# Kernel optimization log

Hardware: AMD Instinct MI355X
Metric: run time of the kernel (lower is better)

The kernel has to match this reference:

```python
import jax, jax.numpy as jnp
import numpy as np

INPUT_DIM = 1024
EMBED_DIM = 256


def setup_inputs() -> dict:
    key = jax.random.key(0)
    ks = jax.random.split(key, 7)
    s_in = 1.0 / np.sqrt(INPUT_DIM)
    x = jax.random.normal(ks[0], (4, 2048, INPUT_DIM), dtype=jnp.float32)
    Wq = jax.random.uniform(ks[1], (INPUT_DIM, EMBED_DIM), jnp.float32, -s_in, s_in)
    bq = jax.random.uniform(ks[2], (EMBED_DIM,), jnp.float32, -s_in, s_in)
    Wk = jax.random.uniform(ks[3], (INPUT_DIM, EMBED_DIM), jnp.float32, -s_in, s_in)
    bk = jax.random.uniform(ks[4], (EMBED_DIM,), jnp.float32, -s_in, s_in)
    Wv = jax.random.uniform(ks[5], (INPUT_DIM, EMBED_DIM), jnp.float32, -s_in, s_in)
    bv = jax.random.uniform(ks[6], (EMBED_DIM,), jnp.float32, -s_in, s_in)
    return {"x": x, "Wq": Wq, "bq": bq, "Wk": Wk, "bk": bk, "Wv": Wv, "bv": bv}


def reference(x, Wq, bq, Wk, bk, Wv, bv):
    # B,T,C -> single-head attention. NOTE: original multiplies by C**0.5.
    C = x.shape[-1]
    scale = jnp.asarray(C, x.dtype) ** 0.5
    q = jnp.einsum('btc,ce->bte', x, Wq) + bq  # [B,T,E]
    k = jnp.einsum('btc,ce->bte', x, Wk) + bk
    v = jnp.einsum('btc,ce->bte', x, Wv) + bv
    wei = jnp.einsum('bqe,bke->bqk', q, k) * scale  # [B,T,T]
    wei = jax.nn.softmax(wei, axis=-1)
    # dropout p=0.0 (eval): identity
    out = jnp.einsum('bqk,bke->bqe', wei, v)  # [B,T,E]
    return out
```

## Files before the change

### kernel.cpp

```cpp
#include <hip/hip_runtime.h>
#include <math.h>

#define IDIM 1024
#define EDIM 256
#define NB 4
#define NT 2048
#define NROW 8192

typedef __attribute__((ext_vector_type(8))) short short8;
typedef __attribute__((ext_vector_type(4))) float f32x4;

#define MFMA16(A,B,C) __builtin_amdgcn_mfma_f32_16x16x32_bf16(A,B,C,0,0,0)
#define GLD16(gsrc, ldst) __builtin_amdgcn_global_load_lds( \
    (const __attribute__((address_space(1))) unsigned int*)(gsrc), \
    (__attribute__((address_space(3))) unsigned int*)(ldst), 16, 0, 0)

__device__ __forceinline__ unsigned short f2bf(float x){
    unsigned u = __builtin_bit_cast(unsigned, x);
    u += 0x7fffu + ((u >> 16) & 1u);
    return (unsigned short)(u >> 16);
}
__device__ __forceinline__ float bf2f(unsigned short h){
    unsigned u = ((unsigned)h) << 16;
    return __builtin_bit_cast(float, u);
}

__global__ __launch_bounds__(256) void split_x(
    const float* __restrict__ X, ushort* __restrict__ Xh, ushort* __restrict__ Xl)
{
    size_t i = ((size_t)blockIdx.x * 256 + threadIdx.x) * 8;
    float4 a = *(const float4*)(X + i);
    float4 b = *(const float4*)(X + i + 4);
    float v[8] = {a.x, a.y, a.z, a.w, b.x, b.y, b.z, b.w};
    union { ushort us[8]; uint4 u; } hi, lo;
    #pragma unroll
    for (int j = 0; j < 8; ++j) {
        unsigned short h = f2bf(v[j]);
        hi.us[j] = h;
        lo.us[j] = f2bf(v[j] - bf2f(h));
    }
    *(uint4*)(Xh + i) = hi.u;
    *(uint4*)(Xl + i) = lo.u;
}

__global__ __launch_bounds__(256) void split_w(
    const float* __restrict__ Wq, const float* __restrict__ Wk, const float* __restrict__ Wv,
    ushort* __restrict__ Wqh, ushort* __restrict__ Wql,
    ushort* __restrict__ Wkh, ushort* __restrict__ Wkl,
    ushort* __restrict__ Wvh)
{
    int u = blockIdx.x * 256 + threadIdx.x;
    int z   = u >> 15;
    int rem = u & 32767;
    int ko  = rem >> 8;
    int e   = rem & 255;
    const float* W = (z == 0) ? Wq : (z == 1) ? Wk : Wv;
    ushort* Oh = (z == 0) ? Wqh : (z == 1) ? Wkh : Wvh;
    ushort* Ol = (z == 0) ? Wql : Wkl;
    union { ushort us[8]; uint4 v; } hi, lo;
    #pragma unroll
    for (int j = 0; j < 8; ++j) {
        float wv = W[(size_t)(ko * 8 + j) * 256 + e];
        unsigned short h = f2bf(wv);
        hi.us[j] = h;
        lo.us[j] = f2bf(wv - bf2f(h));
    }
    *(uint4*)(Oh + (size_t)e * 1024 + ko * 8) = hi.v;
    if (z < 2) *(uint4*)(Ol + (size_t)e * 1024 + ko * 8) = lo.v;
}

__global__ __launch_bounds__(256) void qkv_proj(
    const ushort* __restrict__ Xh, const ushort* __restrict__ Xl,
    const ushort* __restrict__ Whq, const ushort* __restrict__ Wlq,
    const ushort* __restrict__ Whk, const ushort* __restrict__ Wlk,
    const ushort* __restrict__ Whv,
    const float* __restrict__ bq, const float* __restrict__ bk, const float* __restrict__ bv,
    ushort* __restrict__ Qh, ushort* __restrict__ Ql,
    ushort* __restrict__ Kh, ushort* __restrict__ Kl,
    ushort* __restrict__ Vt)
{
    __shared__ ushort Ah[4096], Al[4096], Bh[4096], Bl[4096];

    const int tid = threadIdx.x;
    const int lane = tid & 63, w = tid >> 6;
    const int ln = tid & 15, quad = (tid >> 4) & 3;
    const int wr = w >> 1, wc = w & 1;
    const int z = blockIdx.z;
    const int n0 = blockIdx.x * 128, m0 = blockIdx.y * 128;
    const ushort* Wh = (z == 0) ? Whq : (z == 1) ? Whk : Whv;
    const ushort* Wl = (z == 0) ? Wlq : Wlk;

    f32x4 acc[4][4];
    #pragma unroll
    for (int mi = 0; mi < 4; ++mi)
        #pragma unroll
        for (int ni = 0; ni < 4; ++ni) acc[mi][ni] = (f32x4){0.f, 0.f, 0.f, 0.f};

    const ushort* a0 = Xh + (size_t)(m0 + lane) * IDIM + w * 8;
    const ushort* a1 = Xh + (size_t)(m0 + 64 + lane) * IDIM + w * 8;
    const ushort* a0l = Xl + (size_t)(m0 + lane) * IDIM + w * 8;
    const ushort* a1l = Xl + (size_t)(m0 + 64 + lane) * IDIM + w * 8;
    const ushort* b0 = Wh + (size_t)(n0 + lane) * IDIM + w * 8;
    const ushort* b1 = Wh + (size_t)(n0 + 64 + lane) * IDIM + w * 8;
    const ushort* b0l = Wl + (size_t)(n0 + lane) * IDIM + w * 8;
    const ushort* b1l = Wl + (size_t)(n0 + 64 + lane) * IDIM + w * 8;
    ushort* dA0 = Ah + (size_t)(w * 128) * 8;
    ushort* dA1 = Ah + (size_t)(w * 128 + 64) * 8;
    ushort* dA0l = Al + (size_t)(w * 128) * 8;
    ushort* dA1l = Al + (size_t)(w * 128 + 64) * 8;
    ushort* dB0 = Bh + (size_t)(w * 128) * 8;
    ushort* dB1 = Bh + (size_t)(w * 128 + 64) * 8;
    ushort* dB0l = Bl + (size_t)(w * 128) * 8;
    ushort* dB1l = Bl + (size_t)(w * 128 + 64) * 8;

    for (int kk = 0; kk < IDIM; kk += 32) {
        GLD16(a0 + kk, dA0);
        GLD16(a1 + kk, dA1);
        GLD16(b0 + kk, dB0);
        GLD16(b1 + kk, dB1);
        if (z < 2) {
            GLD16(a0l + kk, dA0l);
            GLD16(a1l + kk, dA1l);
            GLD16(b0l + kk, dB0l);
            GLD16(b1l + kk, dB1l);
        }
        __syncthreads();

        short8 ah[4], al[4], bh[4], bl[4];
        #pragma unroll
        for (int mi = 0; mi < 4; ++mi) {
            int au = quad * 128 + wr * 64 + mi * 16 + ln;
            ah[mi] = *(const short8*)(Ah + au * 8);
            if (z < 2) al[mi] = *(const short8*)(Al + au * 8);
        }
        #pragma unroll
        for (int ni = 0; ni < 4; ++ni) {
            int bu = quad * 128 + wc * 64 + ni * 16 + ln;
            bh[ni] = *(const short8*)(Bh + bu * 8);
            if (z < 2) bl[ni] = *(const short8*)(Bl + bu * 8);
        }
        if (z < 2) {
            #pragma unroll
            for (int ni = 0; ni < 4; ++ni)
                #pragma unroll
                for (int mi = 0; mi < 4; ++mi) {
                    acc[mi][ni] = MFMA16(ah[mi], bh[ni], acc[mi][ni]);
                    acc[mi][ni] = MFMA16(ah[mi], bl[ni], acc[mi][ni]);
                    acc[mi][ni] = MFMA16(al[mi], bh[ni], acc[mi][ni]);
                }
        } else {
            #pragma unroll
            for (int ni = 0; ni < 4; ++ni)
                #pragma unroll
                for (int mi = 0; mi < 4; ++mi)
                    acc[mi][ni] = MFMA16(ah[mi], bh[ni], acc[mi][ni]);
        }
        __syncthreads();
    }

    if (z < 2) {
        ushort* OH = (z == 0) ? Qh : Kh;
        ushort* OL = (z == 0) ? Ql : Kl;
        const float* bias = (z == 0) ? bq : bk;
        const float scale = (z == 0) ? 46.16624130844683f : 1.0f;
        #pragma unroll
        for (int ni = 0; ni < 4; ++ni) {
            int col = n0 + wc * 64 + ni * 16 + ln;
            float bb = bias[col];
            #pragma unroll
            for (int mi = 0; mi < 4; ++mi)
                #pragma unroll
                for (int r = 0; r < 4; ++r) {
                    int row = m0 + wr * 64 + mi * 16 + quad * 4 + r;
                    float v = (acc[mi][ni][r] + bb) * scale;
                    unsigned short hh = f2bf(v);
                    OH[(size_t)row * EDIM + col] = hh;
                    OL[(size_t)row * EDIM + col] = f2bf(v - bf2f(hh));
                }
        }
    } else {
        #pragma unroll
        for (int ni = 0; ni < 4; ++ni) {
            int col = n0 + wc * 64 + ni * 16 + ln;
            float bb = bv[col];
            #pragma unroll
            for (int mi = 0; mi < 4; ++mi) {
                int rowb = m0 + wr * 64 + mi * 16 + quad * 4;
                union { ushort us[4]; uint2 v; } pk;
                #pragma unroll
                for (int r = 0; r < 4; ++r) pk.us[r] = f2bf(acc[mi][ni][r] + bb);
                *(uint2*)(Vt + (size_t)col * NROW + rowb) = pk.v;
            }
        }
    }
}

__global__ __launch_bounds__(256, 2) void attn(
    const ushort* __restrict__ Qh, const ushort* __restrict__ Ql,
    const ushort* __restrict__ Kh, const ushort* __restrict__ Kl,
    const ushort* __restrict__ Vt, ushort* __restrict__ Op, float* __restrict__ mlbuf)
{
    __shared__ ushort KVbuf[4096];
    __shared__ ushort Qls[16384];
    __shared__ ushort Pall[4 * 1088];

    const int tid = threadIdx.x;
    const int lane = tid & 63;
    const int ln = tid & 15, quad = (tid >> 4) & 3, w = tid >> 6;
    ushort* Qls_w = Qls + w * 4096;
    ushort* Pw = Pall + w * 1088;

    const int id = blockIdx.x;
    const int cls = id & 15;
    const int b = cls >> 2, kvq = cls & 3;
    const int qt = id >> 4;
    const int qrow0w = b * NT + qt * 64 + w * 16;
    const int kvbase = b * NT + kvq * 512;

    short8 qh8[8];
    #pragma unroll
    for (int kc = 0; kc < 8; ++kc)
        qh8[kc] = *(const short8*)(Qh + (size_t)(qrow0w + ln) * EDIM + kc * 32 + quad * 8);
    #pragma unroll
    for (int i = 0; i < 8; ++i) {
        int u = i * 64 + lane;
        int ko = u >> 4, ln2 = u & 15;
        *(uint4*)(Qls_w + u * 8) =
            *(const uint4*)(Ql + (size_t)(qrow0w + ln2) * EDIM + ko * 8);
    }

    float m_r[4], l_r[4];
    #pragma unroll
    for (int r = 0; r < 4; ++r) { m_r[r] = -3e38f; l_r[r] = 0.f; }
    f32x4 o[16];
    #pragma unroll
    for (int ni = 0; ni < 16; ++ni) o[ni] = (f32x4){0.f, 0.f, 0.f, 0.f};

    for (int t = 0; t < 8; ++t) {
        const int kv0 = kvbase + t * 64;
        f32x4 s[4];
        #pragma unroll
        for (int ni = 0; ni < 4; ++ni) s[ni] = (f32x4){0.f, 0.f, 0.f, 0.f};

        #pragma unroll
        for (int kc = 0; kc < 8; ++kc) {
            size_t goff = (size_t)(kv0 + w * 16 + (lane & 15)) * EDIM
                          + kc * 32 + (lane >> 4) * 8;
            GLD16(Kh + goff, KVbuf + w * 512);
            GLD16(Kl + goff, KVbuf + 2048 + w * 512);
            __syncthreads();
            short8 ql8 = *(const short8*)(Qls_w + ((kc * 4 + quad) * 16 + ln) * 8);
            #pragma unroll
            for (int ni = 0; ni < 4; ++ni) {
                short8 bh = *(const short8*)(KVbuf + (ni * 64 + quad * 16 + ln) * 8);
                short8 bl = *(const short8*)(KVbuf + 2048 + (ni * 64 + quad * 16 + ln) * 8);
                s[ni] = MFMA16(qh8[kc], bh, s[ni]);
                s[ni] = MFMA16(qh8[kc], bl, s[ni]);
                s[ni] = MFMA16(ql8, bh, s[ni]);
            }
            __syncthreads();
        }

        float mt[4];
        #pragma unroll
        for (int r = 0; r < 4; ++r)
            mt[r] = fmaxf(fmaxf(s[0][r], s[1][r]), fmaxf(s[2][r], s[3][r]));
        #pragma unroll
        for (int mask = 1; mask < 16; mask <<= 1)
            #pragma unroll
            for (int r = 0; r < 4; ++r)
                mt[r] = fmaxf(mt[r], __shfl_xor(mt[r], mask));
        float alpha[4];
        #pragma unroll
        for (int r = 0; r < 4; ++r) {
            float mn = fmaxf(m_r[r], mt[r]);
            alpha[r] = exp2f(m_r[r] - mn);
            m_r[r] = mn;
        }
        float ls[4] = {0.f, 0.f, 0.f, 0.f};
        #pragma unroll
        for (int ni = 0; ni < 4; ++ni) {
            int colb = ni * 16 + ln;
            #pragma unroll
            for (int r = 0; r < 4; ++r) {
                float p = exp2f(s[ni][r] - m_r[r]);
                ls[r] += p;
                Pw[((colb >> 3) * 17 + quad * 4 + r) * 8 + (colb & 7)] = f2bf(p);
            }
        }
        #pragma unroll
        for (int mask = 1; mask < 16; mask <<= 1)
            #pragma unroll
            for (int r = 0; r < 4; ++r)
                ls[r] += __shfl_xor(ls[r], mask);
        #pragma unroll
        for (int r = 0; r < 4; ++r) l_r[r] = l_r[r] * alpha[r] + ls[r];
        #pragma unroll
        for (int ni = 0; ni < 16; ++ni)
            #pragma unroll
            for (int r = 0; r < 4; ++r) o[ni][r] *= alpha[r];

        short8 apk0 = *(const short8*)(Pw + (quad * 17 + ln) * 8);
        short8 apk1 = *(const short8*)(Pw + ((4 + quad) * 17 + ln) * 8);
        #pragma unroll
        for (int vs = 0; vs < 4; ++vs) {
            size_t gv = (size_t)(vs * 64 + w * 16 + (lane & 15)) * NROW
                        + kv0 + (lane >> 4) * 8;
            GLD16(Vt + gv, KVbuf + w * 1024);
            GLD16(Vt + gv + 32, KVbuf + w * 1024 + 512);
            __syncthreads();
            #pragma unroll
            for (int ni = 0; ni < 4; ++ni) {
                short8 v0 = *(const short8*)(KVbuf + (ni * 128 + quad * 16 + ln) * 8);
                short8 v1 = *(const short8*)(KVbuf + (ni * 128 + 64 + quad * 16 + ln) * 8);
                o[vs * 4 + ni] = MFMA16(apk0, v0, o[vs * 4 + ni]);
                o[vs * 4 + ni] = MFMA16(apk1, v1, o[vs * 4 + ni]);
            }
            __syncthreads();
        }
    }

    const int p = (b * 32 + qt) * 4 + kvq;
    if (ln == 0) {
        #pragma unroll
        for (int r = 0; r < 4; ++r) {
            int row = w * 16 + quad * 4 + r;
            *(float2*)(mlbuf + ((size_t)p * 64 + row) * 2) = make_float2(m_r[r], l_r[r]);
        }
    }
    #pragma unroll
    for (int ni = 0; ni < 16; ++ni)
        #pragma unroll
        for (int r = 0; r < 4; ++r) {
            int row = w * 16 + quad * 4 + r;
            Op[(size_t)p * 16384 + row * 256 + ni * 16 + ln] = f2bf(o[ni][r]);
        }
}

__global__ __launch_bounds__(256) void attn_merge(
    const ushort* __restrict__ Op, const float* __restrict__ mlbuf, float* __restrict__ out)
{
    const int bid = blockIdx.x, t = threadIdx.x;
    const int b = bid >> 7, qt = (bid >> 2) & 31, rg = bid & 3;
    const int row = rg * 16 + (t >> 4);
    const int e0 = (t & 15) * 16;
    const int pb = (b * 32 + qt) * 4;
    float mv[4], lv[4];
    float M = -3e38f;
    #pragma unroll
    for (int w2 = 0; w2 < 4; ++w2) {
        float2 ml = *(const float2*)(mlbuf + ((size_t)(pb + w2) * 64 + row) * 2);
        mv[w2] = ml.x; lv[w2] = ml.y;
        M = fmaxf(M, ml.x);
    }
    float sc[4], denom = 0.f;
    #pragma unroll
    for (int w2 = 0; w2 < 4; ++w2) {
        sc[w2] = exp2f(mv[w2] - M);
        denom += sc[w2] * lv[w2];
    }
    float inv = 1.0f / denom;
    #pragma unroll
    for (int w2 = 0; w2 < 4; ++w2) sc[w2] *= inv;

    float acc[16] = {};
    #pragma unroll
    for (int w2 = 0; w2 < 4; ++w2) {
        const ushort* src = Op + (size_t)(pb + w2) * 16384 + row * 256 + e0;
        #pragma unroll
        for (int c = 0; c < 2; ++c) {
            union { ushort us[8]; uint4 v; } u;
            u.v = *(const uint4*)(src + c * 8);
            #pragma unroll
            for (int j = 0; j < 8; ++j)
                acc[c * 8 + j] += sc[w2] * bf2f(u.us[j]);
        }
    }
    float* op = out + ((size_t)b * NT + qt * 64 + row) * EDIM + e0;
    #pragma unroll
    for (int g = 0; g < 4; ++g)
        *(float4*)(op + g * 4) = make_float4(acc[g*4], acc[g*4+1], acc[g*4+2], acc[g*4+3]);
}

extern "C" void kernel_launch(void* const* d_in, const int* in_sizes, int n_in,
                              void* d_out, int out_size, void* d_ws, size_t ws_size,
                              hipStream_t stream) {
    const float* x  = (const float*)d_in[0];
    const float* Wq = (const float*)d_in[1];
    const float* bq = (const float*)d_in[2];
    const float* Wk = (const float*)d_in[3];
    const float* bk = (const float*)d_in[4];
    const float* Wv = (const float*)d_in[5];
    const float* bv = (const float*)d_in[6];
    float* out = (float*)d_out;

    const size_t NX = (size_t)NROW * IDIM;
    const size_t NE = (size_t)NB * NT * EDIM;
    ushort* Xh = (ushort*)d_ws;
    ushort* Xl = Xh + NX;
    ushort* Qh = Xl + NX;
    ushort* Ql = Qh + NE;
    ushort* Kh = Ql + NE;
    ushort* Kl = Kh + NE;
    ushort* Vt = Kl + NE;
    ushort* Wqh = Vt + NE;
    ushort* Wql = Wqh + 256 * 1024;
    ushort* Wkh = Wql + 256 * 1024;
    ushort* Wkl = Wkh + 256 * 1024;
    ushort* Wvh = Wkl + 256 * 1024;
    ushort* Op  = Xh;
    float*  mlb = (float*)(Xh + (size_t)512 * 16384);

    split_x<<<4096, 256, 0, stream>>>(x, Xh, Xl);
    split_w<<<384, 256, 0, stream>>>(Wq, Wk, Wv, Wqh, Wql, Wkh, Wkl, Wvh);
    qkv_proj<<<dim3(2, 64, 3), 256, 0, stream>>>(Xh, Xl, Wqh, Wql, Wkh, Wkl, Wvh,
                                                 bq, bk, bv, Qh, Ql, Kh, Kl, Vt);
    attn<<<512, 256, 0, stream>>>(Qh, Ql, Kh, Kl, Vt, Op, mlb);
    attn_merge<<<512, 256, 0, stream>>>(Op, mlb, out);
}
```

Before: 233.7 us.

## Rewrite attention kernel with 32x32 MFMA tiles and per-tile K/V staging

The attention kernel now runs 2 waves per block, each owning 32 query rows, and uses 32x32x16 bf16 MFMA instead of 16x16x32. Each 32-key tile of K hi/lo and V is loaded into LDS with a single barrier per tile, replacing the per-k-chunk loads and barriers, and the Q hi/lo fragments stay in registers. The aim is to cut synchronisation and LDS staging overhead and to raise MFMA efficiency. In exchange, register pressure rises sharply (two 16-entry Q fragment sets plus 8 f32x16 accumulators), occupancy drops, and the softmax now does a full 32-lane reduction per row. qkv_proj also gets a launch-bounds occupancy hint.

```diff
diff --git a/kernel.cpp b/kernel.cpp
--- a/kernel.cpp
+++ b/kernel.cpp
@@ -9,8 +9,10 @@
 
 typedef __attribute__((ext_vector_type(8))) short short8;
 typedef __attribute__((ext_vector_type(4))) float f32x4;
+typedef __attribute__((ext_vector_type(16))) float f32x16;
 
 #define MFMA16(A,B,C) __builtin_amdgcn_mfma_f32_16x16x32_bf16(A,B,C,0,0,0)
+#define MFMA32(A,B,C) __builtin_amdgcn_mfma_f32_32x32x16_bf16(A,B,C,0,0,0)
 #define GLD16(gsrc, ldst) __builtin_amdgcn_global_load_lds( \
     (const __attribute__((address_space(1))) unsigned int*)(gsrc), \
     (__attribute__((address_space(3))) unsigned int*)(ldst), 16, 0, 0)
@@ -69,7 +71,7 @@
     if (z < 2) *(uint4*)(Ol + (size_t)e * 1024 + ko * 8) = lo.v;
 }
 
-__global__ __launch_bounds__(256) void qkv_proj(
+__global__ __launch_bounds__(256, 2) void qkv_proj(
     const ushort* __restrict__ Xh, const ushort* __restrict__ Xl,
     const ushort* __restrict__ Whq, const ushort* __restrict__ Wlq,
     const ushort* __restrict__ Whk, const ushort* __restrict__ Wlk,
@@ -195,146 +197,141 @@
     }
 }
 
-__global__ __launch_bounds__(256, 2) void attn(
+__global__ __launch_bounds__(128, 1) void attn(
     const ushort* __restrict__ Qh, const ushort* __restrict__ Ql,
     const ushort* __restrict__ Kh, const ushort* __restrict__ Kl,
     const ushort* __restrict__ Vt, ushort* __restrict__ Op, float* __restrict__ mlbuf)
 {
-    __shared__ ushort KVbuf[4096];
-    __shared__ ushort Qls[16384];
-    __shared__ ushort Pall[4 * 1088];
+    __shared__ ushort KhiL[8192];
+    __shared__ ushort KloL[8192];
+    __shared__ ushort VsL[8192];
+    __shared__ ushort Pall[2 * 1152];
 
     const int tid = threadIdx.x;
-    const int lane = tid & 63;
-    const int ln = tid & 15, quad = (tid >> 4) & 3, w = tid >> 6;
-    ushort* Qls_w = Qls + w * 4096;
-    ushort* Pw = Pall + w * 1088;
+    const int lane = tid & 63, w = tid >> 6;
+    const int lm = lane & 31, hh = lane >> 5;
+    ushort* Pw = Pall + w * 1152;
 
     const int id = blockIdx.x;
     const int cls = id & 15;
     const int b = cls >> 2, kvq = cls & 3;
     const int qt = id >> 4;
-    const int qrow0w = b * NT + qt * 64 + w * 16;
+    const int qrow0w = b * NT + qt * 64 + w * 32;
     const int kvbase = b * NT + kvq * 512;
 
-    short8 qh8[8];
-    #pragma unroll
-    for (int kc = 0; kc < 8; ++kc)
-        qh8[kc] = *(const short8*)(Qh + (size_t)(qrow0w + ln) * EDIM + kc * 32 + quad * 8);
-    #pragma unroll
-    for (int i = 0; i < 8; ++i) {
-        int u = i * 64 + lane;
-        int ko = u >> 4, ln2 = u & 15;
-        *(uint4*)(Qls_w + u * 8) =
-            *(const uint4*)(Ql + (size_t)(qrow0w + ln2) * EDIM + ko * 8);
-    }
-
-    float m_r[4], l_r[4];
-    #pragma unroll
-    for (int r = 0; r < 4; ++r) { m_r[r] = -3e38f; l_r[r] = 0.f; }
-    f32x4 o[16];
-    #pragma unroll
-    for (int ni = 0; ni < 16; ++ni) o[ni] = (f32x4){0.f, 0.f, 0.f, 0.f};
-
-    for (int t = 0; t < 8; ++t) {
-        const int kv0 = kvbase + t * 64;
-        f32x4 s[4];
-        #pragma unroll
-        for (int ni = 0; ni < 4; ++ni) s[ni] = (f32x4){0.f, 0.f, 0.f, 0.f};
-
-        #pragma unroll
-        for (int kc = 0; kc < 8; ++kc) {
-            size_t goff = (size_t)(kv0 + w * 16 + (lane & 15)) * EDIM
-                          + kc * 32 + (lane >> 4) * 8;
-            GLD16(Kh + goff, KVbuf + w * 512);
-            GLD16(Kl + goff, KVbuf + 2048 + w * 512);
-            __syncthreads();
-            short8 ql8 = *(const short8*)(Qls_w + ((kc * 4 + quad) * 16 + ln) * 8);
-            #pragma unroll
-            for (int ni = 0; ni < 4; ++ni) {
-                short8 bh = *(const short8*)(KVbuf + (ni * 64 + quad * 16 + ln) * 8);
-                short8 bl = *(const short8*)(KVbuf + 2048 + (ni * 64 + quad * 16 + ln) * 8);
-                s[ni] = MFMA16(qh8[kc], bh, s[ni]);
-                s[ni] = MFMA16(qh8[kc], bl, s[ni]);
-                s[ni] = MFMA16(ql8, bh, s[ni]);
-            }
-            __syncthreads();
-        }
-
-        float mt[4];
-        #pragma unroll
-        for (int r = 0; r < 4; ++r)
-            mt[r] = fmaxf(fmaxf(s[0][r], s[1][r]), fmaxf(s[2][r], s[3][r]));
-        #pragma unroll
-        for (int mask = 1; mask < 16; mask <<= 1)
-            #pragma unroll
-            for (int r = 0; r < 4; ++r)
-                mt[r] = fmaxf(mt[r], __shfl_xor(mt[r], mask));
-        float alpha[4];
-        #pragma unroll
-        for (int r = 0; r < 4; ++r) {
-            float mn = fmaxf(m_r[r], mt[r]);
+    short8 qh[16], ql[16];
+    #pragma unroll
+    for (int kc = 0; kc < 16; ++kc) {
+        size_t qoff = (size_t)(qrow0w + lm) * EDIM + kc * 16 + hh * 8;
+        qh[kc] = *(const short8*)(Qh + qoff);
+        ql[kc] = *(const short8*)(Ql + qoff);
+    }
+
+    float m_r[16], l_r[16];
+    #pragma unroll
+    for (int r = 0; r < 16; ++r) { m_r[r] = -3e38f; l_r[r] = 0.f; }
+    f32x16 o[8];
+    #pragma unroll
+    for (int eb = 0; eb < 8; ++eb)
+        #pragma unroll
+        for (int r = 0; r < 16; ++r) o[eb][r] = 0.f;
+
+    #pragma unroll 1
+    for (int t = 0; t < 16; ++t) {
+        const int kv0 = kvbase + t * 32;
+
+        #pragma unroll
+        for (int j = 0; j < 8; ++j) {
+            int u = (w * 8 + j) * 64 + lane;
+            int eo = u >> 5, c = u & 31;
+            size_t koff = (size_t)(kv0 + c) * EDIM + eo * 8;
+            GLD16(Kh + koff, KhiL + (size_t)(w * 8 + j) * 512);
+            GLD16(Kl + koff, KloL + (size_t)(w * 8 + j) * 512);
+        }
+        #pragma unroll
+        for (int j = 0; j < 8; ++j) {
+            int u = (w * 8 + j) * 64 + lane;
+            int koct = u >> 8, e = u & 255;
+            GLD16(Vt + (size_t)e * NROW + kv0 + koct * 8,
+                  VsL + (size_t)(w * 8 + j) * 512);
+        }
+        __syncthreads();
+
+        f32x16 s;
+        #pragma unroll
+        for (int r = 0; r < 16; ++r) s[r] = 0.f;
+        #pragma unroll
+        for (int kc = 0; kc < 16; ++kc) {
+            int bu = (kc * 2 + hh) * 32 + lm;
+            short8 bh = *(const short8*)(KhiL + bu * 8);
+            short8 bl = *(const short8*)(KloL + bu * 8);
+            s = MFMA32(qh[kc], bh, s);
+            s = MFMA32(qh[kc], bl, s);
+            s = MFMA32(ql[kc], bh, s);
+        }
+
+        float alpha[16], p[16];
+        #pragma unroll
+        for (int r = 0; r < 16; ++r) {
+            float mt = s[r];
+            #pragma unroll
+            for (int mask = 1; mask < 32; mask <<= 1)
+                mt = fmaxf(mt, __shfl_xor(mt, mask));
+            float mn = fmaxf(m_r[r], mt);
             alpha[r] = exp2f(m_r[r] - mn);
             m_r[r] = mn;
-        }
-        float ls[4] = {0.f, 0.f, 0.f, 0.f};
-        #pragma unroll
-        for (int ni = 0; ni < 4; ++ni) {
-            int colb = ni * 16 + ln;
-            #pragma unroll
-            for (int r = 0; r < 4; ++r) {
-                float p = exp2f(s[ni][r] - m_r[r]);
-                ls[r] += p;
-                Pw[((colb >> 3) * 17 + quad * 4 + r) * 8 + (colb & 7)] = f2bf(p);
+            float pv = exp2f(s[r] - mn);
+            p[r] = pv;
+            float ls = pv;
+            #pragma unroll
+            for (int mask = 1; mask < 32; mask <<= 1)
+                ls += __shfl_xor(ls, mask);
+            l_r[r] = l_r[r] * alpha[r] + ls;
+        }
+        #pragma unroll
+        for (int rg = 0; rg < 4; ++rg) {
+            union { ushort us[4]; uint2 v; } pk;
+            #pragma unroll
+            for (int r4 = 0; r4 < 4; ++r4) pk.us[r4] = f2bf(p[rg * 4 + r4]);
+            *(uint2*)(Pw + lm * 36 + rg * 8 + hh * 4) = pk.v;
+        }
+        #pragma unroll
+        for (int eb = 0; eb < 8; ++eb)
+            #pragma unroll
+            for (int r = 0; r < 16; ++r) o[eb][r] *= alpha[r];
+
+        #pragma unroll
+        for (int c = 0; c < 2; ++c) {
+            short8 ap;
+            #pragma unroll
+            for (int j = 0; j < 8; ++j)
+                ((ushort*)&ap)[j] = Pw[(c * 16 + hh * 8 + j) * 36 + lm];
+            #pragma unroll
+            for (int eb = 0; eb < 8; ++eb) {
+                short8 bv8 = *(const short8*)(VsL +
+                    ((size_t)(c * 2 + hh) * 256 + eb * 32 + lm) * 8);
+                o[eb] = MFMA32(ap, bv8, o[eb]);
             }
         }
-        #pragma unroll
-        for (int mask = 1; mask < 16; mask <<= 1)
-            #pragma unroll
-            for (int r = 0; r < 4; ++r)
-                ls[r] += __shfl_xor(ls[r], mask);
-        #pragma unroll
-        for (int r = 0; r < 4; ++r) l_r[r] = l_r[r] * alpha[r] + ls[r];
-        #pragma unroll
-        for (int ni = 0; ni < 16; ++ni)
-            #pragma unroll
-            for (int r = 0; r < 4; ++r) o[ni][r] *= alpha[r];
-
-        short8 apk0 = *(const short8*)(Pw + (quad * 17 + ln) * 8);
-        short8 apk1 = *(const short8*)(Pw + ((4 + quad) * 17 + ln) * 8);
-        #pragma unroll
-        for (int vs = 0; vs < 4; ++vs) {
-            size_t gv = (size_t)(vs * 64 + w * 16 + (lane & 15)) * NROW
-                        + kv0 + (lane >> 4) * 8;
-            GLD16(Vt + gv, KVbuf + w * 1024);
-            GLD16(Vt + gv + 32, KVbuf + w * 1024 + 512);
-            __syncthreads();
-            #pragma unroll
-            for (int ni = 0; ni < 4; ++ni) {
-                short8 v0 = *(const short8*)(KVbuf + (ni * 128 + quad * 16 + ln) * 8);
-                short8 v1 = *(const short8*)(KVbuf + (ni * 128 + 64 + quad * 16 + ln) * 8);
-                o[vs * 4 + ni] = MFMA16(apk0, v0, o[vs * 4 + ni]);
-                o[vs * 4 + ni] = MFMA16(apk1, v1, o[vs * 4 + ni]);
-            }
-            __syncthreads();
-        }
-    }
-
-    const int p = (b * 32 + qt) * 4 + kvq;
-    if (ln == 0) {
-        #pragma unroll
-        for (int r = 0; r < 4; ++r) {
-            int row = w * 16 + quad * 4 + r;
-            *(float2*)(mlbuf + ((size_t)p * 64 + row) * 2) = make_float2(m_r[r], l_r[r]);
-        }
-    }
-    #pragma unroll
-    for (int ni = 0; ni < 16; ++ni)
-        #pragma unroll
-        for (int r = 0; r < 4; ++r) {
-            int row = w * 16 + quad * 4 + r;
-            Op[(size_t)p * 16384 + row * 256 + ni * 16 + ln] = f2bf(o[ni][r]);
-        }
+        __syncthreads();
+    }
+
+    const int pi = (b * 32 + qt) * 4 + kvq;
+    if (lm == 0) {
+        #pragma unroll
+        for (int r = 0; r < 16; ++r) {
+            int row = w * 32 + (r & 3) + 8 * (r >> 2) + 4 * hh;
+            *(float2*)(mlbuf + ((size_t)pi * 64 + row) * 2) = make_float2(m_r[r], l_r[r]);
+        }
+    }
+    #pragma unroll
+    for (int r = 0; r < 16; ++r) {
+        int row = w * 32 + (r & 3) + 8 * (r >> 2) + 4 * hh;
+        ushort* dst = Op + (size_t)pi * 16384 + row * 256 + lm;
+        #pragma unroll
+        for (int eb = 0; eb < 8; ++eb)
+            dst[eb * 32] = f2bf(o[eb][r]);
+    }
 }
 
 __global__ __launch_bounds__(256) void attn_merge(
@@ -415,6 +412,6 @@
     split_w<<<384, 256, 0, stream>>>(Wq, Wk, Wv, Wqh, Wql, Wkh, Wkl, Wvh);
     qkv_proj<<<dim3(2, 64, 3), 256, 0, stream>>>(Xh, Xl, Wqh, Wql, Wkh, Wkl, Wvh,
                                                  bq, bk, bv, Qh, Ql, Kh, Kl, Vt);
-    attn<<<512, 256, 0, stream>>>(Qh, Ql, Kh, Kl, Vt, Op, mlb);
+    attn<<<512, 128, 0, stream>>>(Qh, Ql, Kh, Kl, Vt, Op, mlb);
     attn_merge<<<512, 256, 0, stream>>>(Op, mlb, out);
 }
```

New measurement: 299.6 us. 1.28x slower.

## Stage whole K/V tile per step in attention, cutting barriers per iteration

Applied to the files above, without the earlier changes.

The attention kernel now loads a full 32-key tile of K-hi, K-lo and V into shared memory once per step with a single barrier, instead of staging small chunks with two barriers each. Q-lo fragments are held in registers rather than LDS, and the KV step shrinks from 64 to 32 keys. This is meant to cut synchronisation and LDS traffic, at the cost of more LDS per block, more registers and twice as many softmax rescale steps. The projection kernel also gets a launch bound of two blocks per CU.

```diff
diff --git a/kernel.cpp b/kernel.cpp
--- a/kernel.cpp
+++ b/kernel.cpp
@@ -69,7 +69,7 @@
     if (z < 2) *(uint4*)(Ol + (size_t)e * 1024 + ko * 8) = lo.v;
 }
 
-__global__ __launch_bounds__(256) void qkv_proj(
+__global__ __launch_bounds__(256, 2) void qkv_proj(
     const ushort* __restrict__ Xh, const ushort* __restrict__ Xl,
     const ushort* __restrict__ Whq, const ushort* __restrict__ Wlq,
     const ushort* __restrict__ Whk, const ushort* __restrict__ Wlk,
@@ -200,15 +200,14 @@
     const ushort* __restrict__ Kh, const ushort* __restrict__ Kl,
     const ushort* __restrict__ Vt, ushort* __restrict__ Op, float* __restrict__ mlbuf)
 {
-    __shared__ ushort KVbuf[4096];
-    __shared__ ushort Qls[16384];
-    __shared__ ushort Pall[4 * 1088];
+    __shared__ ushort KhiL[8192];
+    __shared__ ushort KloL[8192];
+    __shared__ ushort VsL[8192];
+    __shared__ ushort Pall[4 * 544];
 
     const int tid = threadIdx.x;
-    const int lane = tid & 63;
     const int ln = tid & 15, quad = (tid >> 4) & 3, w = tid >> 6;
-    ushort* Qls_w = Qls + w * 4096;
-    ushort* Pw = Pall + w * 1088;
+    ushort* Pw = Pall + w * 544;
 
     const int id = blockIdx.x;
     const int cls = id & 15;
@@ -217,16 +216,12 @@
     const int qrow0w = b * NT + qt * 64 + w * 16;
     const int kvbase = b * NT + kvq * 512;
 
-    short8 qh8[8];
-    #pragma unroll
-    for (int kc = 0; kc < 8; ++kc)
-        qh8[kc] = *(const short8*)(Qh + (size_t)(qrow0w + ln) * EDIM + kc * 32 + quad * 8);
-    #pragma unroll
-    for (int i = 0; i < 8; ++i) {
-        int u = i * 64 + lane;
-        int ko = u >> 4, ln2 = u & 15;
-        *(uint4*)(Qls_w + u * 8) =
-            *(const uint4*)(Ql + (size_t)(qrow0w + ln2) * EDIM + ko * 8);
+    short8 qh8[8], ql8[8];
+    #pragma unroll
+    for (int kc = 0; kc < 8; ++kc) {
+        size_t qoff = (size_t)(qrow0w + ln) * EDIM + kc * 32 + quad * 8;
+        qh8[kc] = *(const short8*)(Qh + qoff);
+        ql8[kc] = *(const short8*)(Ql + qoff);
     }
 
     float m_r[4], l_r[4];
@@ -236,35 +231,46 @@
     #pragma unroll
     for (int ni = 0; ni < 16; ++ni) o[ni] = (f32x4){0.f, 0.f, 0.f, 0.f};
 
-    for (int t = 0; t < 8; ++t) {
-        const int kv0 = kvbase + t * 64;
-        f32x4 s[4];
-        #pragma unroll
-        for (int ni = 0; ni < 4; ++ni) s[ni] = (f32x4){0.f, 0.f, 0.f, 0.f};
-
+    #pragma unroll 1
+    for (int t = 0; t < 16; ++t) {
+        const int kv0 = kvbase + t * 32;
+
+        #pragma unroll
+        for (int r = 0; r < 4; ++r) {
+            int u = r * 256 + tid;
+            int c = u & 31, kq = u >> 5;
+            size_t ksrc = (size_t)(kv0 + c) * EDIM + kq * 8;
+            GLD16(Kh + ksrc, KhiL + (size_t)(r * 256 + (tid & ~63)) * 8);
+            GLD16(Kl + ksrc, KloL + (size_t)(r * 256 + (tid & ~63)) * 8);
+        }
+        #pragma unroll
+        for (int r = 0; r < 4; ++r) {
+            int u = r * 256 + tid;
+            int e = u & 255, kq2 = u >> 8;
+            GLD16(Vt + (size_t)e * NROW + kv0 + kq2 * 8,
+                  VsL + (size_t)(r * 256 + (tid & ~63)) * 8);
+        }
+        __syncthreads();
+
+        f32x4 s[2];
+        s[0] = (f32x4){0.f, 0.f, 0.f, 0.f};
+        s[1] = (f32x4){0.f, 0.f, 0.f, 0.f};
         #pragma unroll
         for (int kc = 0; kc < 8; ++kc) {
-            size_t goff = (size_t)(kv0 + w * 16 + (lane & 15)) * EDIM
-                          + kc * 32 + (lane >> 4) * 8;
-            GLD16(Kh + goff, KVbuf + w * 512);
-            GLD16(Kl + goff, KVbuf + 2048 + w * 512);
-            __syncthreads();
-            short8 ql8 = *(const short8*)(Qls_w + ((kc * 4 + quad) * 16 + ln) * 8);
-            #pragma unroll
-            for (int ni = 0; ni < 4; ++ni) {
-                short8 bh = *(const short8*)(KVbuf + (ni * 64 + quad * 16 + ln) * 8);
-                short8 bl = *(const short8*)(KVbuf + 2048 + (ni * 64 + quad * 16 + ln) * 8);
+            int kq = kc * 4 + quad;
+            #pragma unroll
+            for (int ni = 0; ni < 2; ++ni) {
+                short8 bh = *(const short8*)(KhiL + (kq * 32 + ni * 16 + ln) * 8);
+                short8 bl = *(const short8*)(KloL + (kq * 32 + ni * 16 + ln) * 8);
                 s[ni] = MFMA16(qh8[kc], bh, s[ni]);
                 s[ni] = MFMA16(qh8[kc], bl, s[ni]);
-                s[ni] = MFMA16(ql8, bh, s[ni]);
+                s[ni] = MFMA16(ql8[kc], bh, s[ni]);
             }
-            __syncthreads();
         }
 
         float mt[4];
         #pragma unroll
-        for (int r = 0; r < 4; ++r)
-            mt[r] = fmaxf(fmaxf(s[0][r], s[1][r]), fmaxf(s[2][r], s[3][r]));
+        for (int r = 0; r < 4; ++r) mt[r] = fmaxf(s[0][r], s[1][r]);
         #pragma unroll
         for (int mask = 1; mask < 16; mask <<= 1)
             #pragma unroll
@@ -279,7 +285,7 @@
         }
         float ls[4] = {0.f, 0.f, 0.f, 0.f};
         #pragma unroll
-        for (int ni = 0; ni < 4; ++ni) {
+        for (int ni = 0; ni < 2; ++ni) {
             int colb = ni * 16 + ln;
             #pragma unroll
             for (int r = 0; r < 4; ++r) {
@@ -300,24 +306,13 @@
             #pragma unroll
             for (int r = 0; r < 4; ++r) o[ni][r] *= alpha[r];
 
-        short8 apk0 = *(const short8*)(Pw + (quad * 17 + ln) * 8);
-        short8 apk1 = *(const short8*)(Pw + ((4 + quad) * 17 + ln) * 8);
-        #pragma unroll
-        for (int vs = 0; vs < 4; ++vs) {
-            size_t gv = (size_t)(vs * 64 + w * 16 + (lane & 15)) * NROW
-                        + kv0 + (lane >> 4) * 8;
-            GLD16(Vt + gv, KVbuf + w * 1024);
-            GLD16(Vt + gv + 32, KVbuf + w * 1024 + 512);
-            __syncthreads();
-            #pragma unroll
-            for (int ni = 0; ni < 4; ++ni) {
-                short8 v0 = *(const short8*)(KVbuf + (ni * 128 + quad * 16 + ln) * 8);
-                short8 v1 = *(const short8*)(KVbuf + (ni * 128 + 64 + quad * 16 + ln) * 8);
-                o[vs * 4 + ni] = MFMA16(apk0, v0, o[vs * 4 + ni]);
-                o[vs * 4 + ni] = MFMA16(apk1, v1, o[vs * 4 + ni]);
-            }
-            __syncthreads();
-        }
+        short8 ap = *(const short8*)(Pw + (quad * 17 + ln) * 8);
+        #pragma unroll
+        for (int ni = 0; ni < 16; ++ni) {
+            short8 bv8 = *(const short8*)(VsL + (quad * 256 + ni * 16 + ln) * 8);
+            o[ni] = MFMA16(ap, bv8, o[ni]);
+        }
+        __syncthreads();
     }
 
     const int p = (b * 32 + qt) * 4 + kvq;
```

Measured after the change: 220.6 us. 1.06x faster.
